# Kernel tuning notes

Measured on AMD Instinct MI355X. Metric: run time of the kernel, lower is better.

The kernel has to match this reference:

```python
import jax, jax.numpy as jnp
import numpy as np

B, A, UNITS, HID, T = 16, 256, 64, 64, 3


def setup_inputs() -> dict:
    key = jax.random.key(0)
    ks = jax.random.split(key, 16)
    x = jax.random.normal(ks[0], (B, A + 2, A), dtype=jnp.float32)
    # GNN message-passing weights (torch.randn in original)
    W0 = jax.random.normal(ks[1], (1, UNITS), dtype=jnp.float32)
    W1 = jax.random.normal(ks[2], (UNITS, UNITS), dtype=jnp.float32)
    W2 = jax.random.normal(ks[3], (UNITS, UNITS), dtype=jnp.float32)
    W3 = jax.random.normal(ks[4], (1, UNITS), dtype=jnp.float32)
    # fc_a: Linear(64,64)->ReLU->Linear(64,32)->ReLU->Linear(32,1); stored (in,out)
    s = lambda k, i, o: jax.random.uniform(k, (i, o), jnp.float32, -1, 1) / np.sqrt(i)
    sb = lambda k, i, o: jax.random.uniform(k, (o,), jnp.float32, -1, 1) / np.sqrt(i)
    a_w1, a_b1 = s(ks[5], UNITS, HID), sb(ks[6], UNITS, HID)
    a_w2, a_b2 = s(ks[7], HID, HID // 2), sb(ks[8], HID, HID // 2)
    a_w3, a_b3 = s(ks[9], HID // 2, 1), sb(ks[10], HID // 2, 1)
    # fc_v: Linear(64,64)->ReLU->Linear(64,1)
    v_w1, v_b1 = s(ks[11], UNITS, HID), sb(ks[12], UNITS, HID)
    v_w2, v_b2 = s(ks[13], HID, 1), sb(ks[14], HID, 1)
    return dict(x=x, W0=W0, W1=W1, W2=W2, W3=W3,
                a_w1=a_w1, a_b1=a_b1, a_w2=a_w2, a_b2=a_b2, a_w3=a_w3, a_b3=a_b3,
                v_w1=v_w1, v_b1=v_b1, v_w2=v_w2, v_b2=v_b2)


def reference(x, W0, W1, W2, W3,
              a_w1, a_b1, a_w2, a_b2, a_w3, a_b3,
              v_w1, v_b1, v_w2, v_b2):
    n_actions = x.shape[2]                       # A
    cur_sol = x[:, 0, :][..., None]              # [B, A, 1]
    mask = x[:, 1, :]                            # [B, A]
    weights = x[:, 2:n_actions + 2, :]           # [B, A, A]
    adjacent = (weights != 0).astype(jnp.float32)
    embedding = jnp.zeros((x.shape[0], n_actions, UNITS), dtype=jnp.float32)

    # e3 is loop-invariant in math, but original recomputes each step; keep T small python loop (faithful, T=3 static)
    for _ in range(T):
        e1 = cur_sol @ W0                                        # [B,A,1]@[1,U] -> [B,A,U]
        e2 = (adjacent @ embedding / n_actions) @ W1             # [B,A,U]
        # weights.reshape(B,A,A,1) @ W3(1,U) == outer-product broadcast
        e3_ = jnp.sum(jax.nn.relu(weights[..., None] * W3[0]), axis=2) / n_actions  # [B,A,U]
        e3 = e3_ @ W2
        embedding = jax.nn.relu(e1 + e2 + e3)

    # dueling heads
    h = jax.nn.relu(embedding @ a_w1 + a_b1)
    h = jax.nn.relu(h @ a_w2 + a_b2)
    out_a = (h @ a_w3 + a_b3)[..., 0]                            # [B, A]
    hv = jax.nn.relu(embedding @ v_w1 + v_b1)
    out_v = (hv @ v_w2 + v_b2)[..., 0]                           # [B, A]
    out_v = jnp.sum(out_v, axis=1, keepdims=True)                # [B, 1]
    output = out_v + (out_a - jnp.sum(out_a, axis=1, keepdims=True))
    output = output + mask * 10.0                                # hard_mask=False
    return output
```

## Files before the change

### kernel.cpp

```cpp
#include <hip/hip_runtime.h>


#define MC  0x5F3A9C71u
#define MD  0x5F3A9C72u
#define MDN 0x5F3A9C73u

__device__ __forceinline__ float reluf(float v) { return fmaxf(v, 0.f); }

__global__ __launch_bounds__(256) void k_fused(
    const float* __restrict__ x,
    const float* __restrict__ W0, const float* __restrict__ W1,
    const float* __restrict__ W2, const float* __restrict__ W3,
    const float* __restrict__ aw1, const float* __restrict__ ab1,
    const float* __restrict__ aw2, const float* __restrict__ ab2,
    const float* __restrict__ aw3, const float* __restrict__ ab3,
    const float* __restrict__ vw1, const float* __restrict__ vb1,
    const float* __restrict__ vw2, const float* __restrict__ vb2,
    float* __restrict__ oaw, float* __restrict__ ovv,
    unsigned long long* __restrict__ statsg,
    unsigned int* __restrict__ flagg, unsigned int* __restrict__ flag2,
    float* __restrict__ embg, float* __restrict__ out)
{
    __shared__ float awvs[2048 * 4];
    __shared__ float W1s[4096];
    __shared__ float aw2s[64 * 36];
    __shared__ float embsT[64 * 36];
    __shared__ float poss[256], negs[256], css[256];
    __shared__ float W0s[64], P2s[64], N2s[64], Ssh[64], e2c[64];
    __shared__ float wpart[256], npart[256];
    __shared__ float ab1s[64], vb1s[64], vw2s[64], ab2s[32], aw3s[32];
    __shared__ float ab3s[1], vb2s[1], sov[32];
    __shared__ int zw[4];
    __shared__ unsigned int sflags[8];
    __shared__ int zrow[256];
    __shared__ unsigned long long zmsL[1024];

    const float invA = 1.0f / 256.0f;
    const int t = threadIdx.x;
    const int batch = blockIdx.x & 15;
    const int sub   = blockIdx.x >> 4;
    const int obase = sub * 32;

    {
        int r8 = t >> 3, s8 = t & 7;
        int grow = obase + r8;
        const float* rowp = x + ((size_t)batch * 258 + 2 + grow) * 256 + s8 * 32;
        float pp = 0.f, nn = 0.f, mn = 1e30f;
        #pragma unroll
        for (int c = 0; c < 32; c += 4) {
            float4 v = *(const float4*)(rowp + c);
            pp += fmaxf(v.x, 0.f) + fmaxf(v.y, 0.f) + fmaxf(v.z, 0.f) + fmaxf(v.w, 0.f);
            nn += fminf(v.x, 0.f) + fminf(v.y, 0.f) + fminf(v.z, 0.f) + fminf(v.w, 0.f);
            mn = fminf(mn, fminf(fminf(fabsf(v.x), fabsf(v.y)),
                                 fminf(fabsf(v.z), fabsf(v.w))));
        }
        pp += __shfl_xor(pp, 1); pp += __shfl_xor(pp, 2); pp += __shfl_xor(pp, 4);
        nn += __shfl_xor(nn, 1); nn += __shfl_xor(nn, 2); nn += __shfl_xor(nn, 4);
        mn = fminf(mn, __shfl_xor(mn, 1));
        mn = fminf(mn, __shfl_xor(mn, 2));
        mn = fminf(mn, __shfl_xor(mn, 4));
        if (s8 == 0) {
            float2 f2 = make_float2(pp, nn);
            unsigned long long pk;
            __builtin_memcpy(&pk, &f2, 8);
            __hip_atomic_store(&statsg[batch * 256 + grow], pk,
                               __ATOMIC_RELAXED, __HIP_MEMORY_SCOPE_AGENT);
        }
        int z = (s8 == 0 && mn == 0.f) ? 1 : 0;
        unsigned long long b = __ballot(z);
        if ((t & 63) == 0) zw[t >> 6] = (b != 0ull);
    }
    css[t] = x[(size_t)batch * 66048 + t];

    {
        int j = t & 63, mg = t >> 6;
        float pa = 0.f, na = 0.f;
        #pragma unroll
        for (int k = 0; k < 16; ++k) {
            int m = mg * 16 + k;
            float w3 = W3[m];
            float w2 = W2[m * 64 + j];
            pa = fmaf(fmaxf(w3, 0.f), w2, pa);
            na = fmaf(fminf(w3, 0.f), w2, na);
        }
        wpart[mg * 64 + j] = pa;
        npart[mg * 64 + j] = na;
    }
    __syncthreads();
    if (t == 0) {
        unsigned int fv = (zw[0] | zw[1] | zw[2] | zw[3]) ? MD : MC;
        __hip_atomic_store(&flagg[blockIdx.x], fv,
                           __ATOMIC_RELEASE, __HIP_MEMORY_SCOPE_AGENT);
    }
    if (t < 64) {
        P2s[t] = wpart[t] + wpart[64 + t] + wpart[128 + t] + wpart[192 + t];
        N2s[t] = npart[t] + npart[64 + t] + npart[128 + t] + npart[192 + t];
    }

    #pragma unroll
    for (int k = 0; k < 4; ++k) {
        int idx = k * 1024 + t * 4;
        *(float4*)&W1s[idx] = *(const float4*)&W1[idx];
    }
    #pragma unroll
    for (int k = 0; k < 8; ++k) {
        int e = k * 256 + t;
        int m = e >> 5, cgi = e & 31;
        float2 a = *(const float2*)&aw1[m * 64 + 2 * cgi];
        float2 v = *(const float2*)&vw1[m * 64 + 2 * cgi];
        *(float4*)&awvs[e * 4] = make_float4(a.x, a.y, v.x, v.y);
    }
    #pragma unroll
    for (int k = 0; k < 8; ++k) {
        int idx = k * 256 + t;
        aw2s[(idx >> 5) * 36 + (idx & 31)] = aw2[idx];
    }
    if (t < 64) { W0s[t] = W0[t]; ab1s[t] = ab1[t]; vb1s[t] = vb1[t]; vw2s[t] = vw2[t]; }
    if (t >= 64 && t < 96) { ab2s[t - 64] = ab2[t - 64]; aw3s[t - 64] = aw3[t - 64]; }
    if (t == 96) { ab3s[0] = ab3[0]; vb2s[0] = vb2[0]; }

    if (t < 8) {
        const unsigned int* f = &flagg[t * 16 + batch];
        unsigned int v = __hip_atomic_load(f, __ATOMIC_ACQUIRE, __HIP_MEMORY_SCOPE_AGENT);
        while (v != MC && v != MD) {
            __builtin_amdgcn_s_sleep(1);
            v = __hip_atomic_load(f, __ATOMIC_ACQUIRE, __HIP_MEMORY_SCOPE_AGENT);
        }
        sflags[t] = v;
    }
    __syncthreads();
    const int dirty = (sflags[0] == MD) | (sflags[1] == MD) | (sflags[2] == MD) |
                      (sflags[3] == MD) | (sflags[4] == MD) | (sflags[5] == MD) |
                      (sflags[6] == MD) | (sflags[7] == MD);

    {
        unsigned long long pk = __hip_atomic_load(&statsg[batch * 256 + t],
                                 __ATOMIC_RELAXED, __HIP_MEMORY_SCOPE_AGENT);
        float2 f2;
        __builtin_memcpy(&f2, &pk, 8);
        poss[t] = f2.x;
        negs[t] = f2.y;
    }
    __syncthreads();

    if (!dirty) {
        const int j = t & 63, rg = t >> 6;
        const float w0j = W0s[j], p2j = P2s[j], n2j = N2s[j];
        float c_j = 0.f;
        #pragma unroll
        for (int iter = 0; iter < 2; ++iter) {
            float s = 0.f;
            #pragma unroll 8
            for (int k = 0; k < 64; ++k) {
                int i = rg * 64 + k;
                s += reluf(fmaf(css[i], w0j, (poss[i] * p2j + negs[i] * n2j) * invA) + c_j);
            }
            wpart[rg * 64 + j] = s;
            __syncthreads();
            if (t < 64) {
                float S = wpart[t] + wpart[64 + t] + wpart[128 + t] + wpart[192 + t];
                Ssh[t] = S;
                float c = 0.f;
                #pragma unroll 8
                for (int m = 0; m < 64; ++m) c = fmaf(Ssh[m], W1s[m * 64 + t], c);
                e2c[t] = c * invA;
            }
            __syncthreads();
            c_j = e2c[j];
        }
        {
            int r = t & 31, mg = t >> 5;
            int grow = obase + r;
            float cs = css[grow], pi = poss[grow], ni = negs[grow];
            #pragma unroll
            for (int jj = 0; jj < 8; ++jj) {
                int m = mg * 8 + jj;
                embsT[m * 36 + r] = reluf(fmaf(cs, W0s[m],
                                    (pi * P2s[m] + ni * N2s[m]) * invA) + e2c[m]);
            }
        }
    } else {
        {
            const int r4 = t >> 2, sub4 = t & 3;
            #pragma unroll
            for (int p = 0; p < 4; ++p) {
                int row = p * 64 + r4;
                const float* rowp = x + ((size_t)batch * 258 + 2 + row) * 256 + sub4 * 64;
                unsigned long long zm = 0ull;
                for (int c = 0; c < 64; ++c)
                    if (rowp[c] == 0.f) zm |= 1ull << c;
                zmsL[row * 4 + sub4] = zm;
                int zf = (zm != 0ull);
                zf |= __shfl_xor(zf, 1); zf |= __shfl_xor(zf, 2);
                if (sub4 == 0) zrow[row] = zf;
            }
        }
        __syncthreads();
        float* eb0 = embg + (size_t)blockIdx.x * 32768;
        float* eb1 = eb0 + 16384;
        const int r4 = t >> 2, sub4 = t & 3, jb = sub4 * 16;
        #pragma unroll
        for (int p = 0; p < 4; ++p) {
            int row = p * 64 + r4;
            float cs = css[row], pi = poss[row], ni = negs[row];
            #pragma unroll
            for (int q = 0; q < 16; ++q) {
                int jj = jb + q;
                eb0[row * 64 + jj] = reluf(fmaf(cs, W0s[jj],
                                      (pi * P2s[jj] + ni * N2s[jj]) * invA));
            }
        }
        __syncthreads();
        float* cur = eb0; float* nxt = eb1;
        for (int it = 1; it <= 2; ++it) {
            {
                int j = t & 63, rg = t >> 6;
                float s = 0.f;
                for (int k = 0; k < 64; ++k) s += cur[(rg * 64 + k) * 64 + j];
                wpart[rg * 64 + j] = s;
            }
            __syncthreads();
            if (t < 64) {
                float S = wpart[t] + wpart[64 + t] + wpart[128 + t] + wpart[192 + t];
                Ssh[t] = S;
                float c = 0.f;
                for (int m = 0; m < 64; ++m) c = fmaf(Ssh[m], W1s[m * 64 + t], c);
                e2c[t] = c * invA;
            }
            __syncthreads();
            #pragma unroll
            for (int p = 0; p < 4; ++p) {
                int row = p * 64 + r4;
                float cs = css[row], pi = poss[row], ni = negs[row];
                float acc[16];
                #pragma unroll
                for (int q = 0; q < 16; ++q) {
                    int jj = jb + q;
                    acc[q] = fmaf(cs, W0s[jj], (pi * P2s[jj] + ni * N2s[jj]) * invA)
                             + e2c[jj];
                }
                if (zrow[row]) {
                    for (int wd = 0; wd < 4; ++wd) {
                        unsigned long long zm = zmsL[row * 4 + wd];
                        while (zm) {
                            int k = wd * 64 + __builtin_ctzll(zm);
                            zm &= zm - 1;
                            float corr[16];
                            #pragma unroll
                            for (int q = 0; q < 16; ++q) corr[q] = 0.f;
                            for (int m = 0; m < 64; ++m) {
                                float ebm = cur[k * 64 + m];
                                #pragma unroll
                                for (int q = 0; q < 16; ++q)
                                    corr[q] = fmaf(ebm, W1s[m * 64 + jb + q], corr[q]);
                            }
                            #pragma unroll
                            for (int q = 0; q < 16; ++q) acc[q] -= corr[q] * invA;
                        }
                    }
                }
                #pragma unroll
                for (int q = 0; q < 16; ++q)
                    nxt[row * 64 + jb + q] = reluf(acc[q]);
            }
            __syncthreads();
            float* tmp = cur; cur = nxt; nxt = tmp;
        }
        for (int idx = t; idx < 2048; idx += 256) {
            int r = idx & 31, m = idx >> 5;
            embsT[m * 36 + r] = cur[(obase + r) * 64 + m];
        }
    }
    __syncthreads();

    const int cg  = t & 31;
    const int rg4 = t >> 5;
    float aA0x = 0.f, aA0y = 0.f, aA1x = 0.f, aA1y = 0.f;
    float aA2x = 0.f, aA2y = 0.f, aA3x = 0.f, aA3y = 0.f;
    float aV0x = 0.f, aV0y = 0.f, aV1x = 0.f, aV1y = 0.f;
    float aV2x = 0.f, aV2y = 0.f, aV3x = 0.f, aV3y = 0.f;
    for (int m = 0; m < 64; ++m) {
        float4 em = *(const float4*)&embsT[m * 36 + rg4 * 4];
        float4 w  = *(const float4*)&awvs[(m * 32 + cg) * 4];
        aA0x = fmaf(em.x, w.x, aA0x); aA0y = fmaf(em.x, w.y, aA0y);
        aA1x = fmaf(em.y, w.x, aA1x); aA1y = fmaf(em.y, w.y, aA1y);
        aA2x = fmaf(em.z, w.x, aA2x); aA2y = fmaf(em.z, w.y, aA2y);
        aA3x = fmaf(em.w, w.x, aA3x); aA3y = fmaf(em.w, w.y, aA3y);
        aV0x = fmaf(em.x, w.z, aV0x); aV0y = fmaf(em.x, w.w, aV0y);
        aV1x = fmaf(em.y, w.z, aV1x); aV1y = fmaf(em.y, w.w, aV1y);
        aV2x = fmaf(em.z, w.z, aV2x); aV2y = fmaf(em.z, w.w, aV2y);
        aV3x = fmaf(em.w, w.z, aV3x); aV3y = fmaf(em.w, w.w, aV3y);
    }
    float wvx = vw2s[2 * cg], wvy = vw2s[2 * cg + 1];
    float pv0 = fmaf(reluf(aV0x + vb1s[2 * cg]), wvx, reluf(aV0y + vb1s[2 * cg + 1]) * wvy);
    float pv1 = fmaf(reluf(aV1x + vb1s[2 * cg]), wvx, reluf(aV1y + vb1s[2 * cg + 1]) * wvy);
    float pv2 = fmaf(reluf(aV2x + vb1s[2 * cg]), wvx, reluf(aV2y + vb1s[2 * cg + 1]) * wvy);
    float pv3 = fmaf(reluf(aV3x + vb1s[2 * cg]), wvx, reluf(aV3y + vb1s[2 * cg + 1]) * wvy);
    #pragma unroll
    for (int mk = 1; mk <= 16; mk <<= 1) {
        pv0 += __shfl_xor(pv0, mk); pv1 += __shfl_xor(pv1, mk);
        pv2 += __shfl_xor(pv2, mk); pv3 += __shfl_xor(pv3, mk);
    }
    float b0 = ab1s[2 * cg], b1 = ab1s[2 * cg + 1];
    float h00 = reluf(aA0x + b0), h01 = reluf(aA0y + b1);
    float h10 = reluf(aA1x + b0), h11 = reluf(aA1y + b1);
    float h20 = reluf(aA2x + b0), h21 = reluf(aA2y + b1);
    float h30 = reluf(aA3x + b0), h31 = reluf(aA3y + b1);
    __syncthreads();
    float* h1s = embsT;
    *(float2*)&h1s[(rg4 * 4 + 0) * 66 + 2 * cg] = make_float2(h00, h01);
    *(float2*)&h1s[(rg4 * 4 + 1) * 66 + 2 * cg] = make_float2(h10, h11);
    *(float2*)&h1s[(rg4 * 4 + 2) * 66 + 2 * cg] = make_float2(h20, h21);
    *(float2*)&h1s[(rg4 * 4 + 3) * 66 + 2 * cg] = make_float2(h30, h31);
    if (cg == 0) {
        sov[rg4 * 4 + 0] = pv0 + vb2s[0];
        sov[rg4 * 4 + 1] = pv1 + vb2s[0];
        sov[rg4 * 4 + 2] = pv2 + vb2s[0];
        sov[rg4 * 4 + 3] = pv3 + vb2s[0];
    }
    __syncthreads();

    {
        int r = t >> 3, jg = t & 7;
        float c0 = 0.f, c1 = 0.f, c2 = 0.f, c3 = 0.f;
        for (int q = 0; q < 64; ++q) {
            float h = h1s[r * 66 + q];
            float4 w = *(const float4*)&aw2s[q * 36 + jg * 4];
            c0 = fmaf(h, w.x, c0); c1 = fmaf(h, w.y, c1);
            c2 = fmaf(h, w.z, c2); c3 = fmaf(h, w.w, c3);
        }
        float part = reluf(c0 + ab2s[jg * 4 + 0]) * aw3s[jg * 4 + 0];
        part = fmaf(reluf(c1 + ab2s[jg * 4 + 1]), aw3s[jg * 4 + 1], part);
        part = fmaf(reluf(c2 + ab2s[jg * 4 + 2]), aw3s[jg * 4 + 2], part);
        part = fmaf(reluf(c3 + ab2s[jg * 4 + 3]), aw3s[jg * 4 + 3], part);
        part += __shfl_xor(part, 1);
        part += __shfl_xor(part, 2);
        part += __shfl_xor(part, 4);
        if (jg == 0)
            __hip_atomic_store(&oaw[batch * 256 + obase + r], part + ab3s[0],
                               __ATOMIC_RELAXED, __HIP_MEMORY_SCOPE_AGENT);
    }
    if (t < 32)
        __hip_atomic_store(&ovv[batch * 256 + obase + t], sov[t],
                           __ATOMIC_RELAXED, __HIP_MEMORY_SCOPE_AGENT);
    __syncthreads();
    if (t == 0)
        __hip_atomic_store(&flag2[blockIdx.x], MDN,
                           __ATOMIC_RELEASE, __HIP_MEMORY_SCOPE_AGENT);

    if (sub == 0) {
        if (t < 8) {
            const unsigned int* f = &flag2[t * 16 + batch];
            unsigned int v = __hip_atomic_load(f, __ATOMIC_ACQUIRE,
                                               __HIP_MEMORY_SCOPE_AGENT);
            while (v != MDN) {
                __builtin_amdgcn_s_sleep(1);
                v = __hip_atomic_load(f, __ATOMIC_ACQUIRE, __HIP_MEMORY_SCOPE_AGENT);
            }
        }
        __syncthreads();
        float oa = __hip_atomic_load(&oaw[batch * 256 + t],
                                     __ATOMIC_RELAXED, __HIP_MEMORY_SCOPE_AGENT);
        float ov = __hip_atomic_load(&ovv[batch * 256 + t],
                                     __ATOMIC_RELAXED, __HIP_MEMORY_SCOPE_AGENT);
        float sa = oa, sv = ov;
        #pragma unroll
        for (int mk = 1; mk <= 32; mk <<= 1) {
            sa += __shfl_xor(sa, mk);
            sv += __shfl_xor(sv, mk);
        }
        if ((t & 63) == 0) { wpart[t >> 6] = sa; npart[t >> 6] = sv; }
        __syncthreads();
        float sA = wpart[0] + wpart[1] + wpart[2] + wpart[3];
        float sV = npart[0] + npart[1] + npart[2] + npart[3];
        float mask = x[((size_t)batch * 258 + 1) * 256 + t];
        out[batch * 256 + t] = sV + oa - sA + mask * 10.0f;
    }
}

extern "C" void kernel_launch(void* const* d_in, const int* in_sizes, int n_in,
                              void* d_out, int out_size, void* d_ws, size_t ws_size,
                              hipStream_t stream)
{
    (void)in_sizes; (void)n_in; (void)out_size; (void)ws_size;
    const float* x   = (const float*)d_in[0];
    const float* W0  = (const float*)d_in[1];
    const float* W1  = (const float*)d_in[2];
    const float* W2  = (const float*)d_in[3];
    const float* W3  = (const float*)d_in[4];
    const float* aw1 = (const float*)d_in[5];
    const float* ab1 = (const float*)d_in[6];
    const float* aw2 = (const float*)d_in[7];
    const float* ab2 = (const float*)d_in[8];
    const float* aw3 = (const float*)d_in[9];
    const float* ab3 = (const float*)d_in[10];
    const float* vw1 = (const float*)d_in[11];
    const float* vb1 = (const float*)d_in[12];
    const float* vw2 = (const float*)d_in[13];
    const float* vb2 = (const float*)d_in[14];

    float* ws = (float*)d_ws;
    float* oaw   = ws;
    float* ovv   = ws + 4096;
    unsigned long long* statsg = (unsigned long long*)(ws + 8192);
    unsigned int* flagg = (unsigned int*)(ws + 16384);
    unsigned int* flag2 = (unsigned int*)(ws + 16512);
    float* embg  = ws + 16640;

    k_fused<<<128, 256, 0, stream>>>(x, W0, W1, W2, W3,
                                     aw1, ab1, aw2, ab2, aw3, ab3,
                                     vw1, vb1, vw2, vb2,
                                     oaw, ovv, statsg, flagg, flag2,
                                     embg, (float*)d_out);
}
```

Baseline: 23.99 us.

## Double grid to 256 blocks with 16 rows per block

```diff
diff --git a/kernel.cpp b/kernel.cpp
--- a/kernel.cpp
+++ b/kernel.cpp
@@ -24,14 +24,14 @@
     __shared__ float awvs[2048 * 4];
     __shared__ float W1s[4096];
     __shared__ float aw2s[64 * 36];
-    __shared__ float embsT[64 * 36];
+    __shared__ float embsT[64 * 18];
     __shared__ float poss[256], negs[256], css[256];
     __shared__ float W0s[64], P2s[64], N2s[64], Ssh[64], e2c[64];
     __shared__ float wpart[256], npart[256];
     __shared__ float ab1s[64], vb1s[64], vw2s[64], ab2s[32], aw3s[32];
-    __shared__ float ab3s[1], vb2s[1], sov[32];
+    __shared__ float ab3s[1], vb2s[1], sov[16];
     __shared__ int zw[4];
-    __shared__ unsigned int sflags[8];
+    __shared__ unsigned int sflags[16];
     __shared__ int zrow[256];
     __shared__ unsigned long long zmsL[1024];
 
@@ -39,34 +39,37 @@
     const int t = threadIdx.x;
     const int batch = blockIdx.x & 15;
     const int sub   = blockIdx.x >> 4;
-    const int obase = sub * 32;
+    const int obase = sub * 16;
 
     {
-        int r8 = t >> 3, s8 = t & 7;
-        int grow = obase + r8;
-        const float* rowp = x + ((size_t)batch * 258 + 2 + grow) * 256 + s8 * 32;
+        int r16 = t >> 4, s16 = t & 15;
+        int grow = obase + r16;
+        const float* rowp = x + ((size_t)batch * 258 + 2 + grow) * 256 + s16 * 16;
         float pp = 0.f, nn = 0.f, mn = 1e30f;
         #pragma unroll
-        for (int c = 0; c < 32; c += 4) {
+        for (int c = 0; c < 16; c += 4) {
             float4 v = *(const float4*)(rowp + c);
             pp += fmaxf(v.x, 0.f) + fmaxf(v.y, 0.f) + fmaxf(v.z, 0.f) + fmaxf(v.w, 0.f);
             nn += fminf(v.x, 0.f) + fminf(v.y, 0.f) + fminf(v.z, 0.f) + fminf(v.w, 0.f);
             mn = fminf(mn, fminf(fminf(fabsf(v.x), fabsf(v.y)),
                                  fminf(fabsf(v.z), fabsf(v.w))));
         }
-        pp += __shfl_xor(pp, 1); pp += __shfl_xor(pp, 2); pp += __shfl_xor(pp, 4);
-        nn += __shfl_xor(nn, 1); nn += __shfl_xor(nn, 2); nn += __shfl_xor(nn, 4);
+        pp += __shfl_xor(pp, 1); pp += __shfl_xor(pp, 2);
+        pp += __shfl_xor(pp, 4); pp += __shfl_xor(pp, 8);
+        nn += __shfl_xor(nn, 1); nn += __shfl_xor(nn, 2);
+        nn += __shfl_xor(nn, 4); nn += __shfl_xor(nn, 8);
         mn = fminf(mn, __shfl_xor(mn, 1));
         mn = fminf(mn, __shfl_xor(mn, 2));
         mn = fminf(mn, __shfl_xor(mn, 4));
-        if (s8 == 0) {
+        mn = fminf(mn, __shfl_xor(mn, 8));
+        if (s16 == 0) {
             float2 f2 = make_float2(pp, nn);
             unsigned long long pk;
             __builtin_memcpy(&pk, &f2, 8);
             __hip_atomic_store(&statsg[batch * 256 + grow], pk,
                                __ATOMIC_RELAXED, __HIP_MEMORY_SCOPE_AGENT);
         }
-        int z = (s8 == 0 && mn == 0.f) ? 1 : 0;
+        int z = (s16 == 0 && mn == 0.f) ? 1 : 0;
         unsigned long long b = __ballot(z);
         if ((t & 63) == 0) zw[t >> 6] = (b != 0ull);
     }
@@ -119,7 +122,7 @@
     if (t >= 64 && t < 96) { ab2s[t - 64] = ab2[t - 64]; aw3s[t - 64] = aw3[t - 64]; }
     if (t == 96) { ab3s[0] = ab3[0]; vb2s[0] = vb2[0]; }
 
-    if (t < 8) {
+    if (t < 16) {
         const unsigned int* f = &flagg[t * 16 + batch];
         unsigned int v = __hip_atomic_load(f, __ATOMIC_ACQUIRE, __HIP_MEMORY_SCOPE_AGENT);
         while (v != MC && v != MD) {
@@ -129,9 +132,9 @@
         sflags[t] = v;
     }
     __syncthreads();
-    const int dirty = (sflags[0] == MD) | (sflags[1] == MD) | (sflags[2] == MD) |
-                      (sflags[3] == MD) | (sflags[4] == MD) | (sflags[5] == MD) |
-                      (sflags[6] == MD) | (sflags[7] == MD);
+    int dirty = 0;
+    #pragma unroll
+    for (int k = 0; k < 16; ++k) dirty |= (sflags[k] == MD);
 
     {
         unsigned long long pk = __hip_atomic_load(&statsg[batch * 256 + t],
@@ -169,13 +172,13 @@
             c_j = e2c[j];
         }
         {
-            int r = t & 31, mg = t >> 5;
+            int r = t & 15, mg = t >> 4;
             int grow = obase + r;
             float cs = css[grow], pi = poss[grow], ni = negs[grow];
             #pragma unroll
-            for (int jj = 0; jj < 8; ++jj) {
-                int m = mg * 8 + jj;
-                embsT[m * 36 + r] = reluf(fmaf(cs, W0s[m],
+            for (int jj = 0; jj < 4; ++jj) {
+                int m = mg * 4 + jj;
+                embsT[m * 18 + r] = reluf(fmaf(cs, W0s[m],
                                     (pi * P2s[m] + ni * N2s[m]) * invA) + e2c[m]);
             }
         }
@@ -266,81 +269,64 @@
             __syncthreads();
             float* tmp = cur; cur = nxt; nxt = tmp;
         }
-        for (int idx = t; idx < 2048; idx += 256) {
-            int r = idx & 31, m = idx >> 5;
-            embsT[m * 36 + r] = cur[(obase + r) * 64 + m];
+        for (int idx = t; idx < 1024; idx += 256) {
+            int r = idx & 15, m = idx >> 4;
+            embsT[m * 18 + r] = cur[(obase + r) * 64 + m];
         }
     }
     __syncthreads();
 
     const int cg  = t & 31;
-    const int rg4 = t >> 5;
+    const int rg2 = t >> 5;
     float aA0x = 0.f, aA0y = 0.f, aA1x = 0.f, aA1y = 0.f;
-    float aA2x = 0.f, aA2y = 0.f, aA3x = 0.f, aA3y = 0.f;
     float aV0x = 0.f, aV0y = 0.f, aV1x = 0.f, aV1y = 0.f;
-    float aV2x = 0.f, aV2y = 0.f, aV3x = 0.f, aV3y = 0.f;
     for (int m = 0; m < 64; ++m) {
-        float4 em = *(const float4*)&embsT[m * 36 + rg4 * 4];
+        float2 em = *(const float2*)&embsT[m * 18 + rg2 * 2];
         float4 w  = *(const float4*)&awvs[(m * 32 + cg) * 4];
         aA0x = fmaf(em.x, w.x, aA0x); aA0y = fmaf(em.x, w.y, aA0y);
         aA1x = fmaf(em.y, w.x, aA1x); aA1y = fmaf(em.y, w.y, aA1y);
-        aA2x = fmaf(em.z, w.x, aA2x); aA2y = fmaf(em.z, w.y, aA2y);
-        aA3x = fmaf(em.w, w.x, aA3x); aA3y = fmaf(em.w, w.y, aA3y);
         aV0x = fmaf(em.x, w.z, aV0x); aV0y = fmaf(em.x, w.w, aV0y);
         aV1x = fmaf(em.y, w.z, aV1x); aV1y = fmaf(em.y, w.w, aV1y);
-        aV2x = fmaf(em.z, w.z, aV2x); aV2y = fmaf(em.z, w.w, aV2y);
-        aV3x = fmaf(em.w, w.z, aV3x); aV3y = fmaf(em.w, w.w, aV3y);
     }
     float wvx = vw2s[2 * cg], wvy = vw2s[2 * cg + 1];
     float pv0 = fmaf(reluf(aV0x + vb1s[2 * cg]), wvx, reluf(aV0y + vb1s[2 * cg + 1]) * wvy);
     float pv1 = fmaf(reluf(aV1x + vb1s[2 * cg]), wvx, reluf(aV1y + vb1s[2 * cg + 1]) * wvy);
-    float pv2 = fmaf(reluf(aV2x + vb1s[2 * cg]), wvx, reluf(aV2y + vb1s[2 * cg + 1]) * wvy);
-    float pv3 = fmaf(reluf(aV3x + vb1s[2 * cg]), wvx, reluf(aV3y + vb1s[2 * cg + 1]) * wvy);
     #pragma unroll
     for (int mk = 1; mk <= 16; mk <<= 1) {
         pv0 += __shfl_xor(pv0, mk); pv1 += __shfl_xor(pv1, mk);
-        pv2 += __shfl_xor(pv2, mk); pv3 += __shfl_xor(pv3, mk);
     }
     float b0 = ab1s[2 * cg], b1 = ab1s[2 * cg + 1];
     float h00 = reluf(aA0x + b0), h01 = reluf(aA0y + b1);
     float h10 = reluf(aA1x + b0), h11 = reluf(aA1y + b1);
-    float h20 = reluf(aA2x + b0), h21 = reluf(aA2y + b1);
-    float h30 = reluf(aA3x + b0), h31 = reluf(aA3y + b1);
     __syncthreads();
     float* h1s = embsT;
-    *(float2*)&h1s[(rg4 * 4 + 0) * 66 + 2 * cg] = make_float2(h00, h01);
-    *(float2*)&h1s[(rg4 * 4 + 1) * 66 + 2 * cg] = make_float2(h10, h11);
-    *(float2*)&h1s[(rg4 * 4 + 2) * 66 + 2 * cg] = make_float2(h20, h21);
-    *(float2*)&h1s[(rg4 * 4 + 3) * 66 + 2 * cg] = make_float2(h30, h31);
+    *(float2*)&h1s[(rg2 * 2 + 0) * 66 + 2 * cg] = make_float2(h00, h01);
+    *(float2*)&h1s[(rg2 * 2 + 1) * 66 + 2 * cg] = make_float2(h10, h11);
     if (cg == 0) {
-        sov[rg4 * 4 + 0] = pv0 + vb2s[0];
-        sov[rg4 * 4 + 1] = pv1 + vb2s[0];
-        sov[rg4 * 4 + 2] = pv2 + vb2s[0];
-        sov[rg4 * 4 + 3] = pv3 + vb2s[0];
+        sov[rg2 * 2 + 0] = pv0 + vb2s[0];
+        sov[rg2 * 2 + 1] = pv1 + vb2s[0];
     }
     __syncthreads();
 
     {
-        int r = t >> 3, jg = t & 7;
-        float c0 = 0.f, c1 = 0.f, c2 = 0.f, c3 = 0.f;
+        int r = t >> 4, jg = t & 15;
+        float c0 = 0.f, c1 = 0.f;
         for (int q = 0; q < 64; ++q) {
             float h = h1s[r * 66 + q];
-            float4 w = *(const float4*)&aw2s[q * 36 + jg * 4];
+            float2 w = *(const float2*)&aw2s[q * 36 + jg * 2];
             c0 = fmaf(h, w.x, c0); c1 = fmaf(h, w.y, c1);
-            c2 = fmaf(h, w.z, c2); c3 = fmaf(h, w.w, c3);
-        }
-        float part = reluf(c0 + ab2s[jg * 4 + 0]) * aw3s[jg * 4 + 0];
-        part = fmaf(reluf(c1 + ab2s[jg * 4 + 1]), aw3s[jg * 4 + 1], part);
-        part = fmaf(reluf(c2 + ab2s[jg * 4 + 2]), aw3s[jg * 4 + 2], part);
-        part = fmaf(reluf(c3 + ab2s[jg * 4 + 3]), aw3s[jg * 4 + 3], part);
+        }
+        float part = reluf(c0 + ab2s[jg * 2 + 0]) * aw3s[jg * 2 + 0];
+        part = fmaf(reluf(c1 + ab2s[jg * 2 + 1]), aw3s[jg * 2 + 1], part);
         part += __shfl_xor(part, 1);
         part += __shfl_xor(part, 2);
         part += __shfl_xor(part, 4);
+        part += __shfl_xor(part, 8);
         if (jg == 0)
             __hip_atomic_store(&oaw[batch * 256 + obase + r], part + ab3s[0],
                                __ATOMIC_RELAXED, __HIP_MEMORY_SCOPE_AGENT);
     }
-    if (t < 32)
+    if (t < 16)
         __hip_atomic_store(&ovv[batch * 256 + obase + t], sov[t],
                            __ATOMIC_RELAXED, __HIP_MEMORY_SCOPE_AGENT);
     __syncthreads();
@@ -349,7 +335,7 @@
                            __ATOMIC_RELEASE, __HIP_MEMORY_SCOPE_AGENT);
 
     if (sub == 0) {
-        if (t < 8) {
+        if (t < 16) {
             const unsigned int* f = &flag2[t * 16 + batch];
             unsigned int v = __hip_atomic_load(f, __ATOMIC_ACQUIRE,
                                                __HIP_MEMORY_SCOPE_AGENT);
@@ -404,10 +390,10 @@
     float* ovv   = ws + 4096;
     unsigned long long* statsg = (unsigned long long*)(ws + 8192);
     unsigned int* flagg = (unsigned int*)(ws + 16384);
-    unsigned int* flag2 = (unsigned int*)(ws + 16512);
-    float* embg  = ws + 16640;
-
-    k_fused<<<128, 256, 0, stream>>>(x, W0, W1, W2, W3,
+    unsigned int* flag2 = (unsigned int*)(ws + 16640);
+    float* embg  = ws + 17408;
+
+    k_fused<<<256, 256, 0, stream>>>(x, W0, W1, W2, W3,
                                      aw1, ab1, aw2, ab2, aw3, ab3,
                                      vw1, vb1, vw2, vb2,
                                      oaw, ovv, statsg, flagg, flag2,
```

After: 23.44 us (median of 2 runs). -2.3%, faster.
